# Optimization experiments

Hardware: AMD Instinct MI355X
Metric: run time of the kernel (lower is better)

The kernel has to match this reference:

```python
import jax, jax.numpy as jnp
import numpy as np

N_NODES = 100000
N_EDGES = 1600000
D_IN = 128
D_HID = 128
D_OUT = 128


def setup_inputs() -> dict:
    key = jax.random.key(0)
    ks = jax.random.split(key, 8)
    x = jax.random.normal(ks[0], (N_NODES, D_IN), dtype=jnp.float32)
    edge_index = jax.random.randint(ks[1], (2, N_EDGES), 0, N_NODES, dtype=jnp.int64)
    s = 1.0 / np.sqrt(D_IN)
    W1 = jax.random.normal(ks[2], (D_IN, D_HID), dtype=jnp.float32) * s
    W2 = jax.random.normal(ks[3], (D_HID, D_HID), dtype=jnp.float32) * s
    W3 = jax.random.normal(ks[4], (D_HID, D_OUT), dtype=jnp.float32) * s
    b1 = jnp.zeros((D_HID,), jnp.float32)
    b2 = jnp.zeros((D_HID,), jnp.float32)
    b3 = jnp.zeros((D_OUT,), jnp.float32)
    return {"x": x, "edge_index": edge_index, "W1": W1, "b1": b1,
            "W2": W2, "b2": b2, "W3": W3, "b3": b3}


def reference(x, edge_index, W1, b1, W2, b2, W3, b3):
    # PyG GCNConv semantics: add self-loops, symmetric deg^{-1/2} normalization,
    # message = norm * (x W)[src], scatter-add into dst, then + bias; ReLU after each layer.
    n = x.shape[0]
    loops = jnp.arange(n, dtype=edge_index.dtype)
    src = jnp.concatenate([edge_index[0], loops])  # [E+N]
    dst = jnp.concatenate([edge_index[1], loops])  # [E+N]
    deg = jax.ops.segment_sum(jnp.ones_like(dst, dtype=x.dtype), dst, num_segments=n)
    dinv = jnp.where(deg > 0, jax.lax.rsqrt(deg), 0.0)
    norm = (dinv[src] * dinv[dst])[:, None]  # [E+N, 1]

    def layer(h, W, b):
        h = h @ W                                     # [N, d_out] small GEMM
        msg = h[src] * norm                           # gather + scale  [E+N, d_out]
        agg = jax.ops.segment_sum(msg, dst, num_segments=n)  # scatter-add
        return jax.nn.relu(agg + b)

    x = layer(x, W1, b1)
    x = layer(x, W2, b2)
    x = layer(x, W3, b3)
    return x
```

## Files before the change

### kernel.cpp

```cpp
#include <hip/hip_runtime.h>

#define NN 100000
#define NE 1600000
#define DD 128
#define NB 98
#define NGRP 8
#define NPG (NN / NGRP)
#define CSRCAP 1900032
#define NBLK_B 1024
#define EPB 1563
#define BCAP 210000
#define WJ 256
#define NW 49
#define NSUB (NGRP * NW)
#define SCAP 4608
#define LCAP 5632
#define NSLOT 64


typedef __attribute__((ext_vector_type(8))) short short8;
typedef __attribute__((ext_vector_type(4))) float f32x4;

__device__ __forceinline__ unsigned bf16rn(float f) {
  unsigned u = __float_as_uint(f);
  return (u + 0x7fffu + ((u >> 16) & 1u)) >> 16;
}
__device__ __forceinline__ unsigned pk2(float a, float b) {
  return bf16rn(a) | (bf16rn(b) << 16);
}
__device__ __forceinline__ float lo_f(unsigned u) { return __uint_as_float(u << 16); }
__device__ __forceinline__ float hi_f(unsigned u) { return __uint_as_float(u & 0xffff0000u); }


__global__ __launch_bounds__(256) void k_init(int* __restrict__ gcur,
                                              int* __restrict__ scur) {
  int i = blockIdx.x * 256 + threadIdx.x;
  if (i < NGRP) gcur[i] = 0;
  if (i < NSUB) scur[i] = 0;
}

__global__ __launch_bounds__(256) void k_bucket(const void* __restrict__ ei,
                                                int* __restrict__ bpk,
                                                int* __restrict__ gcur) {
  __shared__ int lcnt[4][NGRP], wbase[4][NGRP], lcur[4][NGRP];
  __shared__ int zcnt;
  const int t = threadIdx.x;
  const int wv = t >> 6;
  if (t == 0) zcnt = 0;
  if (t < 4 * NGRP) { ((int*)lcnt)[t] = 0; ((int*)lcur)[t] = 0; }
  __syncthreads();
  if (t < 64) {
    const unsigned* w = (const unsigned*)ei;
    int z = 0;
    for (int i = t; i < 256; i += 64)
      if (w[2 * i + 1] == 0u) z++;
    atomicAdd(&zcnt, z);
  }
  __syncthreads();
  const int isLL = (zcnt >= 250);
  const long long e0 = (long long)blockIdx.x * EPB;
  const int nE = (int)((NE - e0) < EPB ? (NE - e0) : EPB);
  int epk[7], eb[7];
#pragma unroll
  for (int k = 0; k < 7; k++) {
    int idx = t + k * 256;
    eb[k] = -1;
    if (idx < nE) {
      long long e = e0 + idx;
      int s, d;
      if (isLL) {
        s = (int)((const long long*)ei)[e];
        d = (int)((const long long*)ei)[NE + e];
      } else {
        s = ((const int*)ei)[e];
        d = ((const int*)ei)[NE + e];
      }
      int b = d / NPG;
      eb[k] = b;
      epk[k] = s | ((d - b * NPG) << 17);
      atomicAdd(&lcnt[wv][b], 1);
    }
  }
  __syncthreads();
  if (t < NGRP) {
    int c0 = lcnt[0][t], c1 = lcnt[1][t], c2 = lcnt[2][t], c3 = lcnt[3][t];
    int base = atomicAdd(&gcur[t], c0 + c1 + c2 + c3);
    wbase[0][t] = base;
    wbase[1][t] = base + c0;
    wbase[2][t] = base + c0 + c1;
    wbase[3][t] = base + c0 + c1 + c2;
  }
  __syncthreads();
#pragma unroll
  for (int k = 0; k < 7; k++) {
    if (eb[k] >= 0) {
      int p = wbase[wv][eb[k]] + atomicAdd(&lcur[wv][eb[k]], 1);
      bpk[(size_t)eb[k] * BCAP + p] = epk[k];
    }
  }
}

__global__ __launch_bounds__(256) void k_sub(const int* __restrict__ bpk,
                                             const int* __restrict__ gcur,
                                             int* __restrict__ ssub,
                                             int* __restrict__ scur) {
  __shared__ int lcnt[4][NW], wbase[4][NW], lcur[4][NW];
  const int g = blockIdx.x & (NGRP - 1);
  const int s = blockIdx.x >> 3;
  const int n = gcur[g];
  const int chunk = (n + NSLOT - 1) / NSLOT;
  const int e0 = s * chunk;
  const int e1 = min(e0 + chunk, n);
  const int t = threadIdx.x;
  const int wv = t >> 6;
  for (int i = t; i < 4 * NW; i += 256) { ((int*)lcnt)[i] = 0; ((int*)lcur)[i] = 0; }
  __syncthreads();
  const int* pb = bpk + (size_t)g * BCAP;
  for (int i = e0 + t; i < e1; i += 256)
    atomicAdd(&lcnt[wv][pb[i] >> 25], 1);
  __syncthreads();
  if (t < NW) {
    int c0 = lcnt[0][t], c1 = lcnt[1][t], c2 = lcnt[2][t], c3 = lcnt[3][t];
    int base = atomicAdd(&scur[g * NW + t], c0 + c1 + c2 + c3);
    wbase[0][t] = base;
    wbase[1][t] = base + c0;
    wbase[2][t] = base + c0 + c1;
    wbase[3][t] = base + c0 + c1 + c2;
  }
  __syncthreads();
  for (int i = e0 + t; i < e1; i += 256) {
    int pk = pb[i];
    int w = pk >> 25;
    int p = wbase[wv][w] + atomicAdd(&lcur[wv][w], 1);
    ssub[(size_t)(g * NW + w) * SCAP + p] = pk;
  }
}

__global__ __launch_bounds__(256) void k_cnt(const int* __restrict__ ssub,
                                             const int* __restrict__ scur,
                                             int* __restrict__ cnt) {
  __shared__ int lc[WJ];
  const int b = blockIdx.x;
  const int g = b / NW, w = b % NW;
  const int n0 = g * NPG + w * WJ;
  const int wn = min(WJ, NPG - w * WJ);
  const int t = threadIdx.x;
  lc[t] = 0;
  __syncthreads();
  const int m = scur[b];
  const int* sp = ssub + (size_t)b * SCAP;
  for (int e = t; e < m; e += 256)
    atomicAdd(&lc[(sp[e] >> 17) & 255], 1);
  __syncthreads();
  if (t < wn) cnt[n0 + t] = lc[t];
}

__global__ __launch_bounds__(256) void k_dinv(const int* __restrict__ cnt,
                                              float* __restrict__ dinv) {
  int i = blockIdx.x * 256 + threadIdx.x;
  if (i < NN) dinv[i] = rsqrtf((float)(cnt[i] + 1));
}

__global__ __launch_bounds__(256) void k_scan1(const int* __restrict__ cnt,
                                               int* __restrict__ bsums) {
  __shared__ int sd[256];
  const int tid = threadIdx.x;
  const int base = blockIdx.x * 1024;
  int s = 0;
#pragma unroll
  for (int j = 0; j < 4; j++) {
    int i = base + tid * 4 + j;
    if (i < NN) s += (cnt[i] + 3) & ~3;
  }
  sd[tid] = s;
  __syncthreads();
  for (int d = 128; d > 0; d >>= 1) {
    if (tid < d) sd[tid] += sd[tid + d];
    __syncthreads();
  }
  if (tid == 0) bsums[blockIdx.x] = sd[0];
}

__global__ __launch_bounds__(128) void k_scan2(int* __restrict__ bsums,
                                               int* __restrict__ offs) {
  __shared__ int sd[128];
  const int tid = threadIdx.x;
  int v = (tid < NB) ? bsums[tid] : 0;
  sd[tid] = v;
  __syncthreads();
  for (int d = 1; d < 128; d <<= 1) {
    int t = (tid >= d) ? sd[tid - d] : 0;
    __syncthreads();
    sd[tid] += t;
    __syncthreads();
  }
  if (tid < NB) bsums[tid] = sd[tid] - v;
  if (tid == 127) offs[NN] = sd[127];
}

__global__ __launch_bounds__(256) void k_scan3(const int* __restrict__ cnt,
                                               const int* __restrict__ bsums,
                                               int* __restrict__ offs) {
  __shared__ int sd[256];
  const int tid = threadIdx.x;
  const int base = blockIdx.x * 1024;
  int v[4];
  int s = 0;
#pragma unroll
  for (int j = 0; j < 4; j++) {
    int i = base + tid * 4 + j;
    v[j] = (i < NN) ? ((cnt[i] + 3) & ~3) : 0;
    s += v[j];
  }
  sd[tid] = s;
  __syncthreads();
  for (int d = 1; d < 256; d <<= 1) {
    int t = (tid >= d) ? sd[tid - d] : 0;
    __syncthreads();
    if (tid >= d) sd[tid] += t;
    __syncthreads();
  }
  int run = bsums[blockIdx.x] + sd[tid] - s;
#pragma unroll
  for (int j = 0; j < 4; j++) {
    int i = base + tid * 4 + j;
    if (i < NN) offs[i] = run;
    run += v[j];
  }
}

__global__ __launch_bounds__(256) void k_csr(const int* __restrict__ ssub,
                                             const int* __restrict__ scur,
                                             const int* __restrict__ offs,
                                             int* __restrict__ csr) {
  __shared__ int L[LCAP];
  __shared__ int loff[WJ], lcur[WJ];
  __shared__ int sR0, sRlen, sm;
  const int b = blockIdx.x;
  const int g = b / NW, w = b % NW;
  const int n0 = g * NPG + w * WJ;
  const int wn = min(WJ, NPG - w * WJ);
  const int t = threadIdx.x;
  for (int i = t; i < LCAP; i += 256) L[i] = NN;
  if (t == 0) {
    sR0 = offs[n0];
    sRlen = offs[n0 + wn] - sR0;
    sm = scur[b];
  }
  __syncthreads();
  const int R0 = sR0, Rlen = sRlen, m = sm;
  for (int i = t; i < wn; i += 256) {
    loff[i] = offs[n0 + i] - R0;
    lcur[i] = 0;
  }
  __syncthreads();
  const int* sp = ssub + (size_t)b * SCAP;
  for (int e = t; e < m; e += 256) {
    int pk = sp[e];
    int dl = (pk >> 17) & 255;
    int pos = loff[dl] + atomicAdd(&lcur[dl], 1);
    if (pos < LCAP) L[pos] = pk & 0x1FFFF;
  }
  __syncthreads();
  for (int i = t * 4; i < Rlen; i += 1024)
    if (i + 3 < LCAP) *(int4*)(csr + R0 + i) = *(const int4*)&L[i];
}

__global__ __launch_bounds__(256) void k_prepw(const float* __restrict__ Wa,
                                               const float* __restrict__ Wb,
                                               const float* __restrict__ Wc,
                                               unsigned* __restrict__ wt,
                                               unsigned* __restrict__ tbuf) {
  if (blockIdx.x == 0 && threadIdx.x < 64)
    tbuf[(size_t)NN * 64 + threadIdx.x] = 0u;
  int id = blockIdx.x * 256 + threadIdx.x;
  int layer = id >> 13;
  int r = id & 8191;
  int n = r >> 6, kp = r & 63;
  const float* W = (layer == 0) ? Wa : (layer == 1) ? Wb : Wc;
  wt[(size_t)layer * 8192 + n * 64 + kp] =
      pk2(W[(size_t)(2 * kp) * DD + n], W[(size_t)(2 * kp + 1) * DD + n]);
}

template <bool F32SRC>
__global__ __launch_bounds__(256) void k_gemm(const void* __restrict__ Av,
                                              const unsigned* __restrict__ Wg,
                                              const float* __restrict__ dinv,
                                              unsigned* __restrict__ T) {
  __shared__ char lds[49408];
  const int t = threadIdx.x;
  const int row0 = blockIdx.x * 64;
  const int w = t >> 6, l = t & 63;
  const int lm = l & 15, kb = l >> 4;

  {
    int r = t >> 2;
    int gr = row0 + r;
#pragma unroll
    for (int s4 = 0; s4 < 4; s4++) {
      int sg = (t & 3) * 4 + s4;
      uint4 u;
      if (gr < NN) {
        if (F32SRC) {
          const float* ap = (const float*)Av + (size_t)gr * DD + sg * 8;
          float4 f0 = *(const float4*)ap;
          float4 f1 = *(const float4*)(ap + 4);
          u.x = pk2(f0.x, f0.y); u.y = pk2(f0.z, f0.w);
          u.z = pk2(f1.x, f1.y); u.w = pk2(f1.z, f1.w);
        } else {
          u = *(const uint4*)((const unsigned*)Av + (size_t)gr * 64 + sg * 4);
        }
      } else {
        u = make_uint4(0u, 0u, 0u, 0u);
      }
      *(uint4*)(lds + r * 256 + ((sg * 16) ^ ((r & 7) << 4))) = u;
    }
  }
#pragma unroll
  for (int q = 0; q < 8; q++) {
    int e = t * 8 + q;
    int n = e >> 4, sg = e & 15;
    uint4 u = *(const uint4*)(Wg + n * 64 + sg * 4);
    *(uint4*)(lds + 16384 + n * 256 + ((sg * 16) ^ ((n & 7) << 4))) = u;
  }
  if (t < 64) {
    int gr = row0 + t;
    *(float*)(lds + 49152 + t * 4) = (gr < NN) ? dinv[gr] : 0.f;
  }
  __syncthreads();

  f32x4 acc[4][2];
#pragma unroll
  for (int i = 0; i < 4; i++)
#pragma unroll
    for (int j = 0; j < 2; j++) acc[i][j] = (f32x4){0.f, 0.f, 0.f, 0.f};

#pragma unroll
  for (int kk = 0; kk < 4; kk++) {
    const int koff = (kk * 4 + kb) * 16;
    short8 af[4], bf[2];
#pragma unroll
    for (int i = 0; i < 4; i++) {
      int r = i * 16 + lm;
      af[i] = *(const short8*)(lds + r * 256 + (koff ^ ((r & 7) << 4)));
    }
#pragma unroll
    for (int j = 0; j < 2; j++) {
      int n = w * 32 + j * 16 + lm;
      bf[j] = *(const short8*)(lds + 16384 + n * 256 + (koff ^ ((n & 7) << 4)));
    }
#pragma unroll
    for (int i = 0; i < 4; i++)
#pragma unroll
      for (int j = 0; j < 2; j++)
        acc[i][j] = __builtin_amdgcn_mfma_f32_16x16x32_bf16(af[i], bf[j], acc[i][j], 0, 0, 0);
  }

#pragma unroll
  for (int i = 0; i < 4; i++) {
#pragma unroll
    for (int j = 0; j < 2; j++) {
#pragma unroll
      for (int q = 0; q < 4; q++) {
        int rl = i * 16 + (l >> 4) * 4 + q;
        float s = *(const float*)(lds + 49152 + rl * 4);
        float v = acc[i][j][q] * s;
        float nb = __shfl_xor(v, 1);
        if ((l & 1) == 0) {
          int gr = row0 + rl;
          if (gr < NN) {
            int cp = w * 16 + j * 8 + (lm >> 1);
            T[(size_t)gr * 64 + cp] = pk2(v, nb);
          }
        }
      }
    }
  }
}

template <bool BF16OUT>
__global__ __launch_bounds__(256) void k_agg(const unsigned* __restrict__ T,
                                             const int* __restrict__ offs,
                                             const int* __restrict__ csr,
                                             const float* __restrict__ dinv,
                                             const float* __restrict__ bias,
                                             void* __restrict__ outv) {
  const int lane = threadIdx.x & 63;
  const int node = blockIdx.x * 4 + (threadIdx.x >> 6);
  if (node >= NN) return;
  unsigned su = T[(size_t)node * 64 + lane];
  float accx = lo_f(su), accy = hi_f(su);
  int j = offs[node];
  const int end = offs[node + 1];
  for (; j + 16 <= end; j += 16) {
    int4 c0 = *(const int4*)(csr + j);
    int4 c1 = *(const int4*)(csr + j + 4);
    int4 c2 = *(const int4*)(csr + j + 8);
    int4 c3 = *(const int4*)(csr + j + 12);
    unsigned u0 = T[(size_t)c0.x * 64 + lane];
    unsigned u1 = T[(size_t)c0.y * 64 + lane];
    unsigned u2 = T[(size_t)c0.z * 64 + lane];
    unsigned u3 = T[(size_t)c0.w * 64 + lane];
    unsigned u4 = T[(size_t)c1.x * 64 + lane];
    unsigned u5 = T[(size_t)c1.y * 64 + lane];
    unsigned u6 = T[(size_t)c1.z * 64 + lane];
    unsigned u7 = T[(size_t)c1.w * 64 + lane];
    unsigned u8 = T[(size_t)c2.x * 64 + lane];
    unsigned u9 = T[(size_t)c2.y * 64 + lane];
    unsigned ua = T[(size_t)c2.z * 64 + lane];
    unsigned ub = T[(size_t)c2.w * 64 + lane];
    unsigned uc = T[(size_t)c3.x * 64 + lane];
    unsigned ud = T[(size_t)c3.y * 64 + lane];
    unsigned ue = T[(size_t)c3.z * 64 + lane];
    unsigned uf = T[(size_t)c3.w * 64 + lane];
    accx += (((lo_f(u0) + lo_f(u1)) + (lo_f(u2) + lo_f(u3))) +
             ((lo_f(u4) + lo_f(u5)) + (lo_f(u6) + lo_f(u7)))) +
            (((lo_f(u8) + lo_f(u9)) + (lo_f(ua) + lo_f(ub))) +
             ((lo_f(uc) + lo_f(ud)) + (lo_f(ue) + lo_f(uf))));
    accy += (((hi_f(u0) + hi_f(u1)) + (hi_f(u2) + hi_f(u3))) +
             ((hi_f(u4) + hi_f(u5)) + (hi_f(u6) + hi_f(u7)))) +
            (((hi_f(u8) + hi_f(u9)) + (hi_f(ua) + hi_f(ub))) +
             ((hi_f(uc) + hi_f(ud)) + (hi_f(ue) + hi_f(uf))));
  }
  for (; j < end; j += 4) {
    int4 c = *(const int4*)(csr + j);
    unsigned u0 = T[(size_t)c.x * 64 + lane];
    unsigned u1 = T[(size_t)c.y * 64 + lane];
    unsigned u2 = T[(size_t)c.z * 64 + lane];
    unsigned u3 = T[(size_t)c.w * 64 + lane];
    accx += (lo_f(u0) + lo_f(u1)) + (lo_f(u2) + lo_f(u3));
    accy += (hi_f(u0) + hi_f(u1)) + (hi_f(u2) + hi_f(u3));
  }
  float s = dinv[node];
  float2 bb = ((const float2*)bias)[lane];
  float ox = fmaxf(accx * s + bb.x, 0.f);
  float oy = fmaxf(accy * s + bb.y, 0.f);
  if (BF16OUT)
    ((unsigned*)outv)[(size_t)node * 64 + lane] = pk2(ox, oy);
  else
    ((float2*)outv)[(size_t)node * 64 + lane] = make_float2(ox, oy);
}


extern "C" void kernel_launch(void* const* d_in, const int* in_sizes, int n_in,
                              void* d_out, int out_size, void* d_ws, size_t ws_size,
                              hipStream_t stream) {
  const float* x = (const float*)d_in[0];
  const void* ei = (const void*)d_in[1];
  const float* W1 = (const float*)d_in[2];
  const float* b1 = (const float*)d_in[3];
  const float* W2 = (const float*)d_in[4];
  const float* b2 = (const float*)d_in[5];
  const float* W3 = (const float*)d_in[6];
  const float* b3 = (const float*)d_in[7];
  float* out = (float*)d_out;

  char* p = (char*)d_ws;
  auto take = [&](size_t bytes) {
    char* r = p;
    p += (bytes + 1023) & ~(size_t)1023;
    return r;
  };
  int* gcur = (int*)take((size_t)NGRP * 4);
  int* scur = (int*)take((size_t)NSUB * 4);
  int* cnt = (int*)take((size_t)NN * 4);
  int* offs = (int*)take((size_t)(NN + 1) * 4);
  int* bsums = (int*)take((size_t)NB * 4);
  float* dinv = (float*)take((size_t)NN * 4);
  unsigned* wt = (unsigned*)take((size_t)3 * DD * 64 * 4);
  int* csr = (int*)take((size_t)CSRCAP * 4);
  char* regA = (char*)take((size_t)(NN + 1) * 64 * 4);
  unsigned* tbuf = (unsigned*)regA;
  int* ssub = (int*)regA;
  char* regB = (char*)take((size_t)NN * 64 * 4);
  unsigned* hbuf = (unsigned*)regB;
  int* bpk = (int*)regB;

  const int nb_n = (NN + 255) / 256;

  k_init<<<2, 256, 0, stream>>>(gcur, scur);
  k_bucket<<<NBLK_B, 256, 0, stream>>>(ei, bpk, gcur);
  k_sub<<<NGRP * NSLOT, 256, 0, stream>>>(bpk, gcur, ssub, scur);
  k_cnt<<<NSUB, 256, 0, stream>>>(ssub, scur, cnt);
  k_dinv<<<nb_n, 256, 0, stream>>>(cnt, dinv);
  k_scan1<<<NB, 256, 0, stream>>>(cnt, bsums);
  k_scan2<<<1, 128, 0, stream>>>(bsums, offs);
  k_scan3<<<NB, 256, 0, stream>>>(cnt, bsums, offs);
  k_csr<<<NSUB, 256, 0, stream>>>(ssub, scur, offs, csr);
  k_prepw<<<96, 256, 0, stream>>>(W1, W2, W3, wt, tbuf);

  const int gb = (NN + 63) / 64;
  const int ab = (NN + 3) / 4;
  k_gemm<true><<<gb, 256, 0, stream>>>(x, wt, dinv, tbuf);
  k_agg<true><<<ab, 256, 0, stream>>>(tbuf, offs, csr, dinv, b1, hbuf);
  k_gemm<false><<<gb, 256, 0, stream>>>(hbuf, wt + 8192, dinv, tbuf);
  k_agg<true><<<ab, 256, 0, stream>>>(tbuf, offs, csr, dinv, b2, hbuf);
  k_gemm<false><<<gb, 256, 0, stream>>>(hbuf, wt + 16384, dinv, tbuf);
  k_agg<false><<<ab, 256, 0, stream>>>(tbuf, offs, csr, dinv, b3, out);
}
```

Before: 416.0 us.

## Fuse CSR preprocessing kernels and merge init with weight packing

Collapses the count, dinv, three-pass global scan and weight-prep launches into fewer kernels. Per-window counts produce dinv and window sums directly, a single 512-thread scan over the 392 windows gives window bases, and k_csr recounts and scans locally to write per-node offsets. Init and weight packing share one launch. This cuts launch count and the per-node cnt round trip in exchange for recounting edges in k_csr, and the LCAP bounds checks are dropped.

```diff
diff --git a/kernel.cpp b/kernel.cpp
--- a/kernel.cpp
+++ b/kernel.cpp
@@ -3,7 +3,6 @@
 #define NN 100000
 #define NE 1600000
 #define DD 128
-#define NB 98
 #define NGRP 8
 #define NPG (NN / NGRP)
 #define CSRCAP 1900032
@@ -32,11 +31,27 @@
 __device__ __forceinline__ float hi_f(unsigned u) { return __uint_as_float(u & 0xffff0000u); }
 
 
-__global__ __launch_bounds__(256) void k_init(int* __restrict__ gcur,
-                                              int* __restrict__ scur) {
-  int i = blockIdx.x * 256 + threadIdx.x;
-  if (i < NGRP) gcur[i] = 0;
-  if (i < NSUB) scur[i] = 0;
+__global__ __launch_bounds__(256) void k_initw(const float* __restrict__ Wa,
+                                               const float* __restrict__ Wb,
+                                               const float* __restrict__ Wc,
+                                               unsigned* __restrict__ wt,
+                                               unsigned* __restrict__ tbuf,
+                                               int* __restrict__ gcur,
+                                               int* __restrict__ scur) {
+  const int t = threadIdx.x;
+  if (blockIdx.x == 96) {
+    if (t < NGRP) gcur[t] = 0;
+    for (int i = t; i < NSUB; i += 256) scur[i] = 0;
+    if (t < 64) tbuf[(size_t)NN * 64 + t] = 0u;
+    return;
+  }
+  int id = blockIdx.x * 256 + t;
+  int layer = id >> 13;
+  int r = id & 8191;
+  int n = r >> 6, kp = r & 63;
+  const float* W = (layer == 0) ? Wa : (layer == 1) ? Wb : Wc;
+  wt[(size_t)layer * 8192 + n * 64 + kp] =
+      pk2(W[(size_t)(2 * kp) * DD + n], W[(size_t)(2 * kp + 1) * DD + n]);
 }
 
 __global__ __launch_bounds__(256) void k_bucket(const void* __restrict__ ei,
@@ -136,10 +151,12 @@
   }
 }
 
-__global__ __launch_bounds__(256) void k_cnt(const int* __restrict__ ssub,
-                                             const int* __restrict__ scur,
-                                             int* __restrict__ cnt) {
+__global__ __launch_bounds__(256) void k_cntd(const int* __restrict__ ssub,
+                                              const int* __restrict__ scur,
+                                              float* __restrict__ dinv,
+                                              int* __restrict__ wsum) {
   __shared__ int lc[WJ];
+  __shared__ int sd[256];
   const int b = blockIdx.x;
   const int g = b / NW, w = b % NW;
   const int n0 = g * NPG + w * WJ;
@@ -152,134 +169,79 @@
   for (int e = t; e < m; e += 256)
     atomicAdd(&lc[(sp[e] >> 17) & 255], 1);
   __syncthreads();
-  if (t < wn) cnt[n0 + t] = lc[t];
-}
-
-__global__ __launch_bounds__(256) void k_dinv(const int* __restrict__ cnt,
-                                              float* __restrict__ dinv) {
-  int i = blockIdx.x * 256 + threadIdx.x;
-  if (i < NN) dinv[i] = rsqrtf((float)(cnt[i] + 1));
-}
-
-__global__ __launch_bounds__(256) void k_scan1(const int* __restrict__ cnt,
-                                               int* __restrict__ bsums) {
-  __shared__ int sd[256];
-  const int tid = threadIdx.x;
-  const int base = blockIdx.x * 1024;
-  int s = 0;
-#pragma unroll
-  for (int j = 0; j < 4; j++) {
-    int i = base + tid * 4 + j;
-    if (i < NN) s += (cnt[i] + 3) & ~3;
-  }
-  sd[tid] = s;
+  if (t < wn) dinv[n0 + t] = rsqrtf((float)(lc[t] + 1));
+  sd[t] = (t < wn) ? ((lc[t] + 3) & ~3) : 0;
   __syncthreads();
   for (int d = 128; d > 0; d >>= 1) {
-    if (tid < d) sd[tid] += sd[tid + d];
+    if (t < d) sd[t] += sd[t + d];
     __syncthreads();
   }
-  if (tid == 0) bsums[blockIdx.x] = sd[0];
-}
-
-__global__ __launch_bounds__(128) void k_scan2(int* __restrict__ bsums,
+  if (t == 0) wsum[b] = sd[0];
+}
+
+__global__ __launch_bounds__(512) void k_scan2(const int* __restrict__ wsum,
+                                               int* __restrict__ wbase,
                                                int* __restrict__ offs) {
-  __shared__ int sd[128];
-  const int tid = threadIdx.x;
-  int v = (tid < NB) ? bsums[tid] : 0;
-  sd[tid] = v;
-  __syncthreads();
-  for (int d = 1; d < 128; d <<= 1) {
-    int t = (tid >= d) ? sd[tid - d] : 0;
+  __shared__ int sd[512];
+  const int t = threadIdx.x;
+  int v = (t < NSUB) ? wsum[t] : 0;
+  sd[t] = v;
+  __syncthreads();
+  for (int d = 1; d < 512; d <<= 1) {
+    int x = (t >= d) ? sd[t - d] : 0;
     __syncthreads();
-    sd[tid] += t;
+    sd[t] += x;
     __syncthreads();
   }
-  if (tid < NB) bsums[tid] = sd[tid] - v;
-  if (tid == 127) offs[NN] = sd[127];
-}
-
-__global__ __launch_bounds__(256) void k_scan3(const int* __restrict__ cnt,
-                                               const int* __restrict__ bsums,
-                                               int* __restrict__ offs) {
-  __shared__ int sd[256];
-  const int tid = threadIdx.x;
-  const int base = blockIdx.x * 1024;
-  int v[4];
-  int s = 0;
-#pragma unroll
-  for (int j = 0; j < 4; j++) {
-    int i = base + tid * 4 + j;
-    v[j] = (i < NN) ? ((cnt[i] + 3) & ~3) : 0;
-    s += v[j];
-  }
-  sd[tid] = s;
-  __syncthreads();
-  for (int d = 1; d < 256; d <<= 1) {
-    int t = (tid >= d) ? sd[tid - d] : 0;
-    __syncthreads();
-    if (tid >= d) sd[tid] += t;
-    __syncthreads();
-  }
-  int run = bsums[blockIdx.x] + sd[tid] - s;
-#pragma unroll
-  for (int j = 0; j < 4; j++) {
-    int i = base + tid * 4 + j;
-    if (i < NN) offs[i] = run;
-    run += v[j];
-  }
+  if (t < NSUB) wbase[t] = sd[t] - v;
+  if (t == 511) offs[NN] = sd[511];
 }
 
 __global__ __launch_bounds__(256) void k_csr(const int* __restrict__ ssub,
                                              const int* __restrict__ scur,
-                                             const int* __restrict__ offs,
+                                             const int* __restrict__ wbase,
+                                             int* __restrict__ offs,
                                              int* __restrict__ csr) {
   __shared__ int L[LCAP];
-  __shared__ int loff[WJ], lcur[WJ];
-  __shared__ int sR0, sRlen, sm;
+  __shared__ int lc[WJ], lcur[WJ], sc[256];
   const int b = blockIdx.x;
   const int g = b / NW, w = b % NW;
   const int n0 = g * NPG + w * WJ;
   const int wn = min(WJ, NPG - w * WJ);
   const int t = threadIdx.x;
+  lc[t] = 0;
+  lcur[t] = 0;
   for (int i = t; i < LCAP; i += 256) L[i] = NN;
-  if (t == 0) {
-    sR0 = offs[n0];
-    sRlen = offs[n0 + wn] - sR0;
-    sm = scur[b];
-  }
-  __syncthreads();
-  const int R0 = sR0, Rlen = sRlen, m = sm;
-  for (int i = t; i < wn; i += 256) {
-    loff[i] = offs[n0 + i] - R0;
-    lcur[i] = 0;
-  }
-  __syncthreads();
+  __syncthreads();
+  const int m = scur[b];
+  const int R0 = wbase[b];
   const int* sp = ssub + (size_t)b * SCAP;
+  for (int e = t; e < m; e += 256)
+    atomicAdd(&lc[(sp[e] >> 17) & 255], 1);
+  __syncthreads();
+  int v = (lc[t] + 3) & ~3;
+  sc[t] = v;
+  __syncthreads();
+  for (int d = 1; d < 256; d <<= 1) {
+    int x = (t >= d) ? sc[t - d] : 0;
+    __syncthreads();
+    sc[t] += x;
+    __syncthreads();
+  }
+  int excl = sc[t] - v;
+  if (t < wn) offs[n0 + t] = R0 + excl;
+  lc[t] = excl;
+  __syncthreads();
   for (int e = t; e < m; e += 256) {
     int pk = sp[e];
     int dl = (pk >> 17) & 255;
-    int pos = loff[dl] + atomicAdd(&lcur[dl], 1);
-    if (pos < LCAP) L[pos] = pk & 0x1FFFF;
-  }
-  __syncthreads();
+    int pos = lc[dl] + atomicAdd(&lcur[dl], 1);
+    L[pos] = pk & 0x1FFFF;
+  }
+  __syncthreads();
+  const int Rlen = sc[255];
   for (int i = t * 4; i < Rlen; i += 1024)
-    if (i + 3 < LCAP) *(int4*)(csr + R0 + i) = *(const int4*)&L[i];
-}
-
-__global__ __launch_bounds__(256) void k_prepw(const float* __restrict__ Wa,
-                                               const float* __restrict__ Wb,
-                                               const float* __restrict__ Wc,
-                                               unsigned* __restrict__ wt,
-                                               unsigned* __restrict__ tbuf) {
-  if (blockIdx.x == 0 && threadIdx.x < 64)
-    tbuf[(size_t)NN * 64 + threadIdx.x] = 0u;
-  int id = blockIdx.x * 256 + threadIdx.x;
-  int layer = id >> 13;
-  int r = id & 8191;
-  int n = r >> 6, kp = r & 63;
-  const float* W = (layer == 0) ? Wa : (layer == 1) ? Wb : Wc;
-  wt[(size_t)layer * 8192 + n * 64 + kp] =
-      pk2(W[(size_t)(2 * kp) * DD + n], W[(size_t)(2 * kp + 1) * DD + n]);
+    *(int4*)(csr + R0 + i) = *(const int4*)&L[i];
 }
 
 template <bool F32SRC>
@@ -463,9 +425,9 @@
   };
   int* gcur = (int*)take((size_t)NGRP * 4);
   int* scur = (int*)take((size_t)NSUB * 4);
-  int* cnt = (int*)take((size_t)NN * 4);
+  int* wsum = (int*)take((size_t)NSUB * 4);
+  int* wbase = (int*)take((size_t)NSUB * 4);
   int* offs = (int*)take((size_t)(NN + 1) * 4);
-  int* bsums = (int*)take((size_t)NB * 4);
   float* dinv = (float*)take((size_t)NN * 4);
   unsigned* wt = (unsigned*)take((size_t)3 * DD * 64 * 4);
   int* csr = (int*)take((size_t)CSRCAP * 4);
@@ -476,18 +438,12 @@
   unsigned* hbuf = (unsigned*)regB;
   int* bpk = (int*)regB;
 
-  const int nb_n = (NN + 255) / 256;
-
-  k_init<<<2, 256, 0, stream>>>(gcur, scur);
+  k_initw<<<97, 256, 0, stream>>>(W1, W2, W3, wt, tbuf, gcur, scur);
   k_bucket<<<NBLK_B, 256, 0, stream>>>(ei, bpk, gcur);
   k_sub<<<NGRP * NSLOT, 256, 0, stream>>>(bpk, gcur, ssub, scur);
-  k_cnt<<<NSUB, 256, 0, stream>>>(ssub, scur, cnt);
-  k_dinv<<<nb_n, 256, 0, stream>>>(cnt, dinv);
-  k_scan1<<<NB, 256, 0, stream>>>(cnt, bsums);
-  k_scan2<<<1, 128, 0, stream>>>(bsums, offs);
-  k_scan3<<<NB, 256, 0, stream>>>(cnt, bsums, offs);
-  k_csr<<<NSUB, 256, 0, stream>>>(ssub, scur, offs, csr);
-  k_prepw<<<96, 256, 0, stream>>>(W1, W2, W3, wt, tbuf);
+  k_cntd<<<NSUB, 256, 0, stream>>>(ssub, scur, dinv, wsum);
+  k_scan2<<<1, 512, 0, stream>>>(wsum, wbase, offs);
+  k_csr<<<NSUB, 256, 0, stream>>>(ssub, scur, wbase, offs, csr);
 
   const int gb = (NN + 63) / 64;
   const int ab = (NN + 3) / 4;
```

Result: faster. 406.3 us (-2.3%).
